# Optimization experiments

Hardware: AMD Instinct MI355X
Metric: run time of the kernel (lower is better)

## Reference

```python
import jax, jax.numpy as jnp
import numpy as np

E, D, H, K, T = 16, 1024, 2048, 2, 2048


def setup_inputs() -> dict:
    key = jax.random.key(0)
    k = jax.random.split(key, 7)
    scale = 0.02
    return {
        "inp": jax.random.normal(k[0], (T, D), dtype=jnp.float32),
        "gate_idx": jax.random.randint(k[1], (T, K), 0, E, dtype=jnp.int64),
        "gate_score": jax.random.uniform(k[2], (T, K), dtype=jnp.float32),
        "w1": jax.random.normal(k[3], (E, H, D), dtype=jnp.float32) * scale,
        "b1": jnp.zeros((E, H), dtype=jnp.float32),
        "w2": jax.random.normal(k[4], (E, D, H), dtype=jnp.float32) * scale,
        "b2": jnp.zeros((E, D), dtype=jnp.float32),
    }


def reference(inp, gate_idx, gate_score, w1, b1, w2, b2):
    num_expert = w1.shape[0]
    top_k = gate_idx.shape[1]
    d_model = inp.shape[1]
    # expand each token top_k times (repeat_interleave along dim 0)
    x = jnp.repeat(inp, top_k, axis=0)           # [T*K, D]
    g = gate_idx.reshape(-1)                      # [T*K]
    o = jnp.zeros((x.shape[0], d_model), dtype=x.dtype)
    # static loop over experts; output masked by expert assignment (same math
    # as the per-expert gather/scatter in the original)
    for i in range(num_expert):
        h = jax.nn.gelu(x @ w1[i].T + b1[i])      # [T*K, H]
        y = h @ w2[i].T + b2[i]                   # [T*K, D]
        o = o + jnp.where((g == i)[:, None], y, jnp.zeros((), x.dtype))
    # combine top_k expert outputs with gate scores (bmm in the original)
    out = jnp.einsum("nk,nkd->nd", gate_score, o.reshape(-1, top_k, d_model))
    return out
```

## Files before the change

kernel.cpp:

```cpp
#include <hip/hip_runtime.h>
#include <hip/hip_bf16.h>
#include <stdint.h>


#define E_ 16
#define D_ 1024
#define H_ 2048
#define K_ 2
#define T_ 2048
#define NP_ (T_ * K_)
#define MTS_ 48

using short8 = __attribute__((ext_vector_type(8))) short;
using f32x4  = __attribute__((ext_vector_type(4))) float;

__device__ __forceinline__ unsigned short f2bf(float f) {
  union { float f; unsigned u; } x; x.f = f;
  unsigned r = x.u + 0x7fffu + ((x.u >> 16) & 1u);
  return (unsigned short)(r >> 16);
}

__device__ __forceinline__ float gelu_f(float x) {
  float u = 1.5957691216057308f * (x + 0.044715f * x * x * x);
  return x / (1.f + __expf(-u));
}

__device__ __forceinline__ void waitv8() {
  asm volatile("s_waitcnt vmcnt(8)" ::: "memory");
  __builtin_amdgcn_sched_barrier(0);
}
__device__ __forceinline__ void waitv0() {
  asm volatile("s_waitcnt vmcnt(0)" ::: "memory");
  __builtin_amdgcn_sched_barrier(0);
}
__device__ __forceinline__ void barrier_only() {
  __builtin_amdgcn_sched_barrier(0);
  __builtin_amdgcn_s_barrier();
  __builtin_amdgcn_sched_barrier(0);
}
__device__ __forceinline__ void lgkm0_barrier() {
  asm volatile("s_waitcnt lgkmcnt(0)" ::: "memory");
  __builtin_amdgcn_sched_barrier(0);
  __builtin_amdgcn_s_barrier();
  __builtin_amdgcn_sched_barrier(0);
}

__global__ void cvt_kernel(const float* __restrict__ src,
                           unsigned short* __restrict__ dst, int n4) {
  int stride = gridDim.x * blockDim.x;
  for (int i = blockIdx.x * blockDim.x + threadIdx.x; i < n4; i += stride) {
    float4 v = reinterpret_cast<const float4*>(src)[i];
    ushort4 o = make_ushort4(f2bf(v.x), f2bf(v.y), f2bf(v.z), f2bf(v.w));
    reinterpret_cast<ushort4*>(dst)[i] = o;
  }
}

__global__ void route_kernel(const int* __restrict__ gidx,
                             int* __restrict__ rows,
                             int* __restrict__ offsets,
                             int2* __restrict__ tiles) {
  __shared__ int cnt[E_], cur[E_];
  int tid = threadIdx.x;
  if (tid < E_) cnt[tid] = 0;
  __syncthreads();
  for (int p = tid; p < NP_; p += blockDim.x) atomicAdd(&cnt[gidx[p]], 1);
  __syncthreads();
  if (tid == 0) {
    int acc = 0;
    for (int e = 0; e < E_; ++e) { offsets[e] = acc; cur[e] = acc; acc += cnt[e]; }
    offsets[E_] = acc;
    int k = 0;
    for (int e = 0; e < E_; ++e)
      for (int m = offsets[e]; m < offsets[e] + cnt[e]; m += 128)
        tiles[k++] = make_int2(e, m);
    for (; k < MTS_; ++k) tiles[k] = make_int2(-1, 0);
  }
  __syncthreads();
  for (int p = tid; p < NP_; p += blockDim.x) {
    int e = gidx[p];
    int pos = atomicAdd(&cur[e], 1);
    rows[pos] = p;
  }
}

#define GLOAD16(g, l)                                                        \
  __builtin_amdgcn_global_load_lds(                                          \
      (const __attribute__((address_space(1))) unsigned int*)(const void*)(g), \
      (__attribute__((address_space(3))) unsigned int*)(void*)(l), 16, 0, 0)

template<bool IS1>
__global__ __launch_bounds__(256, 3)
void moe_gemm(const unsigned short* __restrict__ A0,
              const float* __restrict__ W,
              const float* __restrict__ bias,
              const int* __restrict__ rows,
              const int* __restrict__ offsets,
              const int2* __restrict__ tiles,
              const float* __restrict__ score,
              unsigned short* __restrict__ Hout,
              float* __restrict__ Yout)
{
  constexpr int BM = 128, BN = 64, BK = 64;
  constexpr int KD = IS1 ? D_ : H_;
  constexpr int NN = IS1 ? H_ : D_;
  constexpr int NT = KD / BK;

  const int2 tile = tiles[blockIdx.y];
  const int e = tile.x;
  if (e < 0) return;
  const int s0   = tile.y;
  const int send = offsets[e + 1];
  const int n0   = blockIdx.x * BN;

  __shared__ unsigned short As[2][BM][BK];
  __shared__ unsigned short Bs[2][BN][BK];
  __shared__ int rowsrc[BM];
  __shared__ int rowdst[BM];

  const int tid  = threadIdx.x;
  const int lane = tid & 63;
  const int wid  = tid >> 6;

  if (tid < BM) {
    int s = s0 + tid;
    bool v = s < send;
    int sc2 = v ? s : s0;
    if (IS1) {
      rowsrc[tid] = rows[sc2] >> 1;
      rowdst[tid] = v ? s : -1;
    } else {
      rowsrc[tid] = sc2;
      rowdst[tid] = v ? rows[s] : -1;
    }
  }
  __syncthreads();

  const int arow  = lane >> 3;
  const int aslot = (lane & 7) ^ arow;
  const unsigned short* gA[4];
#pragma unroll
  for (int i = 0; i < 4; ++i)
    gA[i] = A0 + (size_t)rowsrc[wid * 32 + i * 8 + arow] * KD + aslot * 8;

  const int brow = tid >> 3;
  const int boct = tid & 7;
  const float* gB0 = W + (size_t)e * NN * KD + (size_t)(n0 + brow) * KD + boct * 4;
  const float* gB2 = gB0 + (size_t)32 * KD;

  const int wr = wid >> 1, wc = wid & 1;
  const int fr = lane & 15, fh = lane >> 4;

  f32x4 acc[4][2] = {};
  float4 breg0[4], breg1[4];

  auto issueA = [&](int buf, int kk) {
#pragma unroll
    for (int i = 0; i < 4; ++i)
      GLOAD16(gA[i] + kk, &As[buf][wid * 32 + i * 8][0]);
  };
  auto issueB = [&](float4* br, int kk) {
    br[0] = *reinterpret_cast<const float4*>(gB0 + kk);
    br[1] = *reinterpret_cast<const float4*>(gB0 + kk + 32);
    br[2] = *reinterpret_cast<const float4*>(gB2 + kk);
    br[3] = *reinterpret_cast<const float4*>(gB2 + kk + 32);
  };
  auto writeB = [&](int buf, const float4* br) {
#pragma unroll
    for (int p = 0; p < 4; ++p) {
      int row = (p & 2) ? brow + 32 : brow;
      int kl0 = boct * 4 + ((p & 1) ? 32 : 0);
      ushort4 u;
      const float* f = &br[p].x;
      u.x = f2bf(f[0]); u.y = f2bf(f[1]); u.z = f2bf(f[2]); u.w = f2bf(f[3]);
      int idx = (((kl0 >> 3) ^ (row & 7)) << 3) + (kl0 & 7);
      *reinterpret_cast<ushort4*>(&Bs[buf][row][idx]) = u;
    }
  };
  auto compute = [&](int buf) {
    short8 af[4][2], bv[2][2];
#pragma unroll
    for (int mi = 0; mi < 4; ++mi) {
      const int row = wr * 64 + mi * 16 + fr;
#pragma unroll
      for (int ks = 0; ks < 2; ++ks) {
        const int slot = (ks * 4 + fh) ^ (row & 7);
        af[mi][ks] = *reinterpret_cast<const short8*>(&As[buf][row][slot * 8]);
      }
    }
#pragma unroll
    for (int ni = 0; ni < 2; ++ni) {
      const int row = wc * 32 + ni * 16 + fr;
#pragma unroll
      for (int ks = 0; ks < 2; ++ks) {
        const int slot = (ks * 4 + fh) ^ (row & 7);
        bv[ni][ks] = *reinterpret_cast<const short8*>(&Bs[buf][row][slot * 8]);
      }
    }
#pragma unroll
    for (int ks = 0; ks < 2; ++ks)
#pragma unroll
      for (int mi = 0; mi < 4; ++mi)
#pragma unroll
        for (int ni = 0; ni < 2; ++ni)
          acc[mi][ni] = __builtin_amdgcn_mfma_f32_16x16x32_bf16(
              af[mi][ks], bv[ni][ks], acc[mi][ni], 0, 0, 0);
  };

  issueA(0, 0);       issueB(breg0, 0);
  issueA(1, BK);      issueB(breg1, BK);
  waitv8();
  writeB(0, breg0);
  lgkm0_barrier();

  for (int t = 0; t < NT; t += 2) {
    compute(0);
    barrier_only();
    if (t + 2 < NT) {
      issueA(0, (t + 2) * BK); issueB(breg0, (t + 2) * BK);
      waitv8();
    } else {
      waitv0();
    }
    writeB(1, breg1);
    lgkm0_barrier();
    compute(1);
    barrier_only();
    if (t + 2 < NT) {
      if (t + 3 < NT) { issueA(1, (t + 3) * BK); issueB(breg1, (t + 3) * BK); waitv8(); }
      else            { waitv0(); }
      writeB(0, breg0);
      lgkm0_barrier();
    }
  }

  const float* biasE = bias + (size_t)e * NN + n0;
#pragma unroll
  for (int mi = 0; mi < 4; ++mi) {
#pragma unroll
    for (int j = 0; j < 4; ++j) {
      int rt  = wr * 64 + mi * 16 + fh * 4 + j;
      int dst = rowdst[rt];
      if (dst < 0) continue;
      float sc = IS1 ? 0.f : score[dst];
#pragma unroll
      for (int ni = 0; ni < 2; ++ni) {
        int col = wc * 32 + ni * 16 + fr;
        float v = acc[mi][ni][j] + biasE[col];
        if (IS1) {
          Hout[(size_t)dst * H_ + n0 + col] = f2bf(gelu_f(v));
        } else {
          Yout[(size_t)dst * D_ + n0 + col] = v * sc;
        }
      }
    }
  }
}

__global__ void combine_kernel(const float* __restrict__ y,
                               float* __restrict__ out) {
  const int DQ = D_ / 4;
  int i = blockIdx.x * blockDim.x + threadIdx.x;
  int t = i / DQ, d = i % DQ;
  const float4* y4 = reinterpret_cast<const float4*>(y);
  float4 a = y4[(size_t)(2 * t) * DQ + d];
  float4 b = y4[(size_t)(2 * t + 1) * DQ + d];
  reinterpret_cast<float4*>(out)[i] =
      make_float4(a.x + b.x, a.y + b.y, a.z + b.z, a.w + b.w);
}

extern "C" void kernel_launch(void* const* d_in, const int* in_sizes, int n_in,
                              void* d_out, int out_size, void* d_ws, size_t ws_size,
                              hipStream_t stream) {
  const float* inp    = (const float*)d_in[0];
  const int*   gidx   = (const int*)d_in[1];
  const float* gscore = (const float*)d_in[2];
  const float* w1     = (const float*)d_in[3];
  const float* b1     = (const float*)d_in[4];
  const float* w2     = (const float*)d_in[5];
  const float* b2     = (const float*)d_in[6];
  float* out = (float*)d_out;

  char* ws = (char*)d_ws;
  size_t o = 0;
  auto alloc = [&](size_t bytes) {
    void* p = ws + o;
    o = (o + bytes + 255) & ~(size_t)255;
    return p;
  };
  unsigned short* xb   = (unsigned short*)alloc((size_t)T_ * D_ * 2);
  unsigned short* hbuf = (unsigned short*)alloc((size_t)NP_ * H_ * 2);
  float*          ybuf = (float*)alloc((size_t)NP_ * D_ * 4);
  int*            rows = (int*)alloc(NP_ * 4);
  int*         offsets = (int*)alloc((E_ + 1) * 4);
  int2*          tiles = (int2*)alloc(MTS_ * 8);

  cvt_kernel<<<dim3(512), dim3(256), 0, stream>>>(inp, xb, T_ * D_ / 4);
  route_kernel<<<dim3(1), dim3(256), 0, stream>>>(gidx, rows, offsets, tiles);

  moe_gemm<true><<<dim3(H_ / 64, MTS_), dim3(256), 0, stream>>>(
      xb, w1, b1, rows, offsets, tiles, gscore, hbuf, (float*)nullptr);
  moe_gemm<false><<<dim3(D_ / 64, MTS_), dim3(256), 0, stream>>>(
      hbuf, w2, b2, rows, offsets, tiles, gscore, (unsigned short*)nullptr, ybuf);

  combine_kernel<<<dim3(T_ * D_ / 4 / 256), dim3(256), 0, stream>>>(ybuf, out);
}
```

Before: 147.3 us.

## Shrink GEMM K-tile to 32, halve BN for second GEMM, raise occupancy

```diff
diff --git a/kernel.cpp b/kernel.cpp
--- a/kernel.cpp
+++ b/kernel.cpp
@@ -25,8 +25,12 @@
   return x / (1.f + __expf(-u));
 }
 
-__device__ __forceinline__ void waitv8() {
-  asm volatile("s_waitcnt vmcnt(8)" ::: "memory");
+__device__ __forceinline__ void waitv4() {
+  asm volatile("s_waitcnt vmcnt(4)" ::: "memory");
+  __builtin_amdgcn_sched_barrier(0);
+}
+__device__ __forceinline__ void waitv3() {
+  asm volatile("s_waitcnt vmcnt(3)" ::: "memory");
   __builtin_amdgcn_sched_barrier(0);
 }
 __device__ __forceinline__ void waitv0() {
@@ -89,7 +93,7 @@
       (__attribute__((address_space(3))) unsigned int*)(void*)(l), 16, 0, 0)
 
 template<bool IS1>
-__global__ __launch_bounds__(256, 3)
+__global__ __launch_bounds__(256, IS1 ? 5 : 6)
 void moe_gemm(const unsigned short* __restrict__ A0,
               const float* __restrict__ W,
               const float* __restrict__ bias,
@@ -100,7 +104,10 @@
               unsigned short* __restrict__ Hout,
               float* __restrict__ Yout)
 {
-  constexpr int BM = 128, BN = 64, BK = 64;
+  constexpr int BM = 128, BK = 32;
+  constexpr int BN = IS1 ? 64 : 32;
+  constexpr int NI = BN / 32;
+  constexpr int WN = BN / 2;
   constexpr int KD = IS1 ? D_ : H_;
   constexpr int NN = IS1 ? H_ : D_;
   constexpr int NT = KD / BK;
@@ -113,7 +120,7 @@
   const int n0   = blockIdx.x * BN;
 
   __shared__ unsigned short As[2][BM][BK];
-  __shared__ unsigned short Bs[2][BN][BK];
+  __shared__ unsigned short Bs[2][BN][BK + 8];
   __shared__ int rowsrc[BM];
   __shared__ int rowdst[BM];
 
@@ -135,80 +142,67 @@
   }
   __syncthreads();
 
-  const int arow  = lane >> 3;
-  const int aslot = (lane & 7) ^ arow;
-  const unsigned short* gA[4];
-#pragma unroll
-  for (int i = 0; i < 4; ++i)
-    gA[i] = A0 + (size_t)rowsrc[wid * 32 + i * 8 + arow] * KD + aslot * 8;
-
-  const int brow = tid >> 3;
-  const int boct = tid & 7;
+  const int arow16 = lane >> 2;
+  const int aslot  = (lane & 3) ^ ((arow16 >> 1) & 3);
+  const unsigned short* gA[2];
+#pragma unroll
+  for (int i = 0; i < 2; ++i)
+    gA[i] = A0 + (size_t)rowsrc[wid * 32 + i * 16 + arow16] * KD + aslot * 8;
+
+  const int brow = tid >> 3, boct = tid & 7;
   const float* gB0 = W + (size_t)e * NN * KD + (size_t)(n0 + brow) * KD + boct * 4;
   const float* gB2 = gB0 + (size_t)32 * KD;
 
   const int wr = wid >> 1, wc = wid & 1;
   const int fr = lane & 15, fh = lane >> 4;
 
-  f32x4 acc[4][2] = {};
-  float4 breg0[4], breg1[4];
+  f32x4 acc[4][NI] = {};
+  float4 breg0[2], breg1[2];
 
   auto issueA = [&](int buf, int kk) {
 #pragma unroll
-    for (int i = 0; i < 4; ++i)
-      GLOAD16(gA[i] + kk, &As[buf][wid * 32 + i * 8][0]);
+    for (int i = 0; i < 2; ++i)
+      GLOAD16(gA[i] + kk, &As[buf][wid * 32 + i * 16][0]);
   };
   auto issueB = [&](float4* br, int kk) {
     br[0] = *reinterpret_cast<const float4*>(gB0 + kk);
-    br[1] = *reinterpret_cast<const float4*>(gB0 + kk + 32);
-    br[2] = *reinterpret_cast<const float4*>(gB2 + kk);
-    br[3] = *reinterpret_cast<const float4*>(gB2 + kk + 32);
+    if (IS1) br[1] = *reinterpret_cast<const float4*>(gB2 + kk);
   };
   auto writeB = [&](int buf, const float4* br) {
 #pragma unroll
-    for (int p = 0; p < 4; ++p) {
-      int row = (p & 2) ? brow + 32 : brow;
-      int kl0 = boct * 4 + ((p & 1) ? 32 : 0);
+    for (int p = 0; p < (IS1 ? 2 : 1); ++p) {
+      int row = brow + p * 32;
       ushort4 u;
       const float* f = &br[p].x;
       u.x = f2bf(f[0]); u.y = f2bf(f[1]); u.z = f2bf(f[2]); u.w = f2bf(f[3]);
-      int idx = (((kl0 >> 3) ^ (row & 7)) << 3) + (kl0 & 7);
-      *reinterpret_cast<ushort4*>(&Bs[buf][row][idx]) = u;
+      *reinterpret_cast<ushort4*>(&Bs[buf][row][boct * 4]) = u;
     }
   };
   auto compute = [&](int buf) {
-    short8 af[4][2], bv[2][2];
+    short8 af[4], bv[NI];
 #pragma unroll
     for (int mi = 0; mi < 4; ++mi) {
       const int row = wr * 64 + mi * 16 + fr;
-#pragma unroll
-      for (int ks = 0; ks < 2; ++ks) {
-        const int slot = (ks * 4 + fh) ^ (row & 7);
-        af[mi][ks] = *reinterpret_cast<const short8*>(&As[buf][row][slot * 8]);
-      }
-    }
-#pragma unroll
-    for (int ni = 0; ni < 2; ++ni) {
-      const int row = wc * 32 + ni * 16 + fr;
-#pragma unroll
-      for (int ks = 0; ks < 2; ++ks) {
-        const int slot = (ks * 4 + fh) ^ (row & 7);
-        bv[ni][ks] = *reinterpret_cast<const short8*>(&Bs[buf][row][slot * 8]);
-      }
-    }
-#pragma unroll
-    for (int ks = 0; ks < 2; ++ks)
-#pragma unroll
-      for (int mi = 0; mi < 4; ++mi)
-#pragma unroll
-        for (int ni = 0; ni < 2; ++ni)
-          acc[mi][ni] = __builtin_amdgcn_mfma_f32_16x16x32_bf16(
-              af[mi][ks], bv[ni][ks], acc[mi][ni], 0, 0, 0);
-  };
+      const int slot = fh ^ ((row >> 1) & 3);
+      af[mi] = *reinterpret_cast<const short8*>(&As[buf][row][slot * 8]);
+    }
+#pragma unroll
+    for (int ni = 0; ni < NI; ++ni) {
+      const int row = wc * WN + ni * 16 + fr;
+      bv[ni] = *reinterpret_cast<const short8*>(&Bs[buf][row][fh * 8]);
+    }
+#pragma unroll
+    for (int mi = 0; mi < 4; ++mi)
+#pragma unroll
+      for (int ni = 0; ni < NI; ++ni)
+        acc[mi][ni] = __builtin_amdgcn_mfma_f32_16x16x32_bf16(
+            af[mi], bv[ni], acc[mi][ni], 0, 0, 0);
+  };
+  auto waitNV = [&]() { if (IS1) waitv4(); else waitv3(); };
 
   issueA(0, 0);       issueB(breg0, 0);
   issueA(1, BK);      issueB(breg1, BK);
-  waitv8();
+  waitNV();
   writeB(0, breg0);
   lgkm0_barrier();
 
@@ -217,7 +211,7 @@
     barrier_only();
     if (t + 2 < NT) {
       issueA(0, (t + 2) * BK); issueB(breg0, (t + 2) * BK);
-      waitv8();
+      waitNV();
     } else {
       waitv0();
     }
@@ -226,7 +220,7 @@
     compute(1);
     barrier_only();
     if (t + 2 < NT) {
-      if (t + 3 < NT) { issueA(1, (t + 3) * BK); issueB(breg1, (t + 3) * BK); waitv8(); }
+      if (t + 3 < NT) { issueA(1, (t + 3) * BK); issueB(breg1, (t + 3) * BK); waitNV(); }
       else            { waitv0(); }
       writeB(0, breg0);
       lgkm0_barrier();
@@ -243,8 +237,8 @@
       if (dst < 0) continue;
       float sc = IS1 ? 0.f : score[dst];
 #pragma unroll
-      for (int ni = 0; ni < 2; ++ni) {
-        int col = wc * 32 + ni * 16 + fr;
+      for (int ni = 0; ni < NI; ++ni) {
+        int col = wc * WN + ni * 16 + fr;
         float v = acc[mi][ni][j] + biasE[col];
         if (IS1) {
           Hout[(size_t)dst * H_ + n0 + col] = f2bf(gelu_f(v));
@@ -299,7 +293,7 @@
 
   moe_gemm<true><<<dim3(H_ / 64, MTS_), dim3(256), 0, stream>>>(
       xb, w1, b1, rows, offsets, tiles, gscore, hbuf, (float*)nullptr);
-  moe_gemm<false><<<dim3(D_ / 64, MTS_), dim3(256), 0, stream>>>(
+  moe_gemm<false><<<dim3(D_ / 32, MTS_), dim3(256), 0, stream>>>(
       hbuf, w2, b2, rows, offsets, tiles, gscore, (unsigned short*)nullptr, ybuf);
 
   combine_kernel<<<dim3(T_ * D_ / 4 / 256), dim3(256), 0, stream>>>(ybuf, out);
```

Result: slower. 186.4 us (+26.5%).

## Fuse both expert GEMMs into one launch with per-tile completion counters

Applied to the files above, without the earlier changes.

```diff
diff --git a/kernel.cpp b/kernel.cpp
--- a/kernel.cpp
+++ b/kernel.cpp
@@ -58,20 +58,22 @@
 __global__ void route_kernel(const int* __restrict__ gidx,
                              int* __restrict__ rows,
                              int* __restrict__ offsets,
-                             int2* __restrict__ tiles) {
-  __shared__ int cnt[E_], cur[E_];
+                             int2* __restrict__ tiles,
+                             int* __restrict__ cnt) {
+  __shared__ int c[E_], cur[E_];
   int tid = threadIdx.x;
-  if (tid < E_) cnt[tid] = 0;
+  if (tid < E_) c[tid] = 0;
+  if (tid < MTS_) cnt[tid] = 0;
   __syncthreads();
-  for (int p = tid; p < NP_; p += blockDim.x) atomicAdd(&cnt[gidx[p]], 1);
+  for (int p = tid; p < NP_; p += blockDim.x) atomicAdd(&c[gidx[p]], 1);
   __syncthreads();
   if (tid == 0) {
     int acc = 0;
-    for (int e = 0; e < E_; ++e) { offsets[e] = acc; cur[e] = acc; acc += cnt[e]; }
+    for (int e = 0; e < E_; ++e) { offsets[e] = acc; cur[e] = acc; acc += c[e]; }
     offsets[E_] = acc;
     int k = 0;
     for (int e = 0; e < E_; ++e)
-      for (int m = offsets[e]; m < offsets[e] + cnt[e]; m += 128)
+      for (int m = offsets[e]; m < offsets[e] + c[e]; m += 128)
         tiles[k++] = make_int2(e, m);
     for (; k < MTS_; ++k) tiles[k] = make_int2(-1, 0);
   }
@@ -88,29 +90,37 @@
       (const __attribute__((address_space(1))) unsigned int*)(const void*)(g), \
       (__attribute__((address_space(3))) unsigned int*)(void*)(l), 16, 0, 0)
 
-template<bool IS1>
 __global__ __launch_bounds__(256, 3)
-void moe_gemm(const unsigned short* __restrict__ A0,
-              const float* __restrict__ W,
-              const float* __restrict__ bias,
-              const int* __restrict__ rows,
-              const int* __restrict__ offsets,
-              const int2* __restrict__ tiles,
-              const float* __restrict__ score,
-              unsigned short* __restrict__ Hout,
-              float* __restrict__ Yout)
+void moe_fused(const unsigned short* __restrict__ xb,
+               unsigned short* __restrict__ hbuf,
+               const float* __restrict__ w1,
+               const float* __restrict__ w2,
+               const float* __restrict__ b1,
+               const float* __restrict__ b2,
+               const int* __restrict__ rows,
+               const int* __restrict__ offsets,
+               const int2* __restrict__ tiles,
+               const float* __restrict__ score,
+               int* __restrict__ cnt,
+               float* __restrict__ ybuf)
 {
   constexpr int BM = 128, BN = 64, BK = 64;
-  constexpr int KD = IS1 ? D_ : H_;
-  constexpr int NN = IS1 ? H_ : D_;
-  constexpr int NT = KD / BK;
 
   const int2 tile = tiles[blockIdx.y];
   const int e = tile.x;
   if (e < 0) return;
+  const bool is1 = blockIdx.x < 32;
+  const int nb   = is1 ? blockIdx.x : (blockIdx.x - 32);
+  const int KD   = is1 ? D_ : H_;
+  const int NN   = is1 ? H_ : D_;
+  const int NT   = is1 ? (D_ / BK) : (H_ / BK);
+  const float* W    = is1 ? w1 : w2;
+  const float* bias = is1 ? b1 : b2;
+  const unsigned short* A0 = is1 ? xb : hbuf;
+
   const int s0   = tile.y;
   const int send = offsets[e + 1];
-  const int n0   = blockIdx.x * BN;
+  const int n0   = nb * BN;
 
   __shared__ unsigned short As[2][BM][BK];
   __shared__ unsigned short Bs[2][BN][BK];
@@ -121,11 +131,19 @@
   const int lane = tid & 63;
   const int wid  = tid >> 6;
 
+  if (!is1) {
+    if (tid == 0) {
+      while (atomicAdd(&cnt[blockIdx.y], 0) < 32) __builtin_amdgcn_s_sleep(8);
+    }
+    __syncthreads();
+    __builtin_amdgcn_fence(__ATOMIC_ACQUIRE, "agent");
+  }
+
   if (tid < BM) {
     int s = s0 + tid;
     bool v = s < send;
     int sc2 = v ? s : s0;
-    if (IS1) {
+    if (is1) {
       rowsrc[tid] = rows[sc2] >> 1;
       rowdst[tid] = v ? s : -1;
     } else {
@@ -142,8 +160,7 @@
   for (int i = 0; i < 4; ++i)
     gA[i] = A0 + (size_t)rowsrc[wid * 32 + i * 8 + arow] * KD + aslot * 8;
 
-  const int brow = tid >> 3;
-  const int boct = tid & 7;
+  const int brow = tid >> 3, boct = tid & 7;
   const float* gB0 = W + (size_t)e * NN * KD + (size_t)(n0 + brow) * KD + boct * 4;
   const float* gB2 = gB0 + (size_t)32 * KD;
 
@@ -241,17 +258,26 @@
       int rt  = wr * 64 + mi * 16 + fh * 4 + j;
       int dst = rowdst[rt];
       if (dst < 0) continue;
-      float sc = IS1 ? 0.f : score[dst];
+      float sc = is1 ? 0.f : score[dst];
 #pragma unroll
       for (int ni = 0; ni < 2; ++ni) {
         int col = wc * 32 + ni * 16 + fr;
         float v = acc[mi][ni][j] + biasE[col];
-        if (IS1) {
-          Hout[(size_t)dst * H_ + n0 + col] = f2bf(gelu_f(v));
+        if (is1) {
+          hbuf[(size_t)dst * H_ + n0 + col] = f2bf(gelu_f(v));
         } else {
-          Yout[(size_t)dst * D_ + n0 + col] = v * sc;
+          ybuf[(size_t)dst * D_ + n0 + col] = v * sc;
         }
       }
+    }
+  }
+
+  if (is1) {
+    asm volatile("s_waitcnt vmcnt(0)" ::: "memory");
+    __syncthreads();
+    if (tid == 0) {
+      __builtin_amdgcn_fence(__ATOMIC_RELEASE, "agent");
+      atomicAdd(&cnt[blockIdx.y], 1);
     }
   }
 }
@@ -293,14 +319,13 @@
   int*            rows = (int*)alloc(NP_ * 4);
   int*         offsets = (int*)alloc((E_ + 1) * 4);
   int2*          tiles = (int2*)alloc(MTS_ * 8);
+  int*             cnt = (int*)alloc(MTS_ * 4);
 
   cvt_kernel<<<dim3(512), dim3(256), 0, stream>>>(inp, xb, T_ * D_ / 4);
-  route_kernel<<<dim3(1), dim3(256), 0, stream>>>(gidx, rows, offsets, tiles);
-
-  moe_gemm<true><<<dim3(H_ / 64, MTS_), dim3(256), 0, stream>>>(
-      xb, w1, b1, rows, offsets, tiles, gscore, hbuf, (float*)nullptr);
-  moe_gemm<false><<<dim3(D_ / 64, MTS_), dim3(256), 0, stream>>>(
-      hbuf, w2, b2, rows, offsets, tiles, gscore, (unsigned short*)nullptr, ybuf);
+  route_kernel<<<dim3(1), dim3(256), 0, stream>>>(gidx, rows, offsets, tiles, cnt);
+
+  moe_fused<<<dim3(48, MTS_), dim3(256), 0, stream>>>(
+      xb, hbuf, w1, w2, b1, b2, rows, offsets, tiles, gscore, cnt, ybuf);
 
   combine_kernel<<<dim3(T_ * D_ / 4 / 256), dim3(256), 0, stream>>>(ybuf, out);
 }
```

Measured after the change: 332.0 us. +125.4%, slower.
